# Performance work log

Hardware: AMD Instinct MI355X
Metric: run time of the kernel (lower is better)

Reference implementation:

```python
import jax, jax.numpy as jnp
import numpy as np

V, E, H2, K = 30000, 256, 256, 13  # vocab, embed dim, per-direction hidden, num tags
B, T = 64, 512


def setup_inputs() -> dict:
    key = jax.random.key(0)
    ks = jax.random.split(key, 12)
    s = 0.1
    return {
        "x": jax.random.randint(ks[0], (B, T), 0, V, dtype=jnp.int32),
        "emb": jax.random.normal(ks[1], (V, E), dtype=jnp.float32) * s,
        "w_ih_f": jax.random.normal(ks[2], (4 * H2, E), dtype=jnp.float32) * s,
        "w_hh_f": jax.random.normal(ks[3], (4 * H2, H2), dtype=jnp.float32) * s,
        "b_ih_f": jnp.zeros((4 * H2,), jnp.float32),
        "b_hh_f": jnp.zeros((4 * H2,), jnp.float32),
        "w_ih_b": jax.random.normal(ks[4], (4 * H2, E), dtype=jnp.float32) * s,
        "w_hh_b": jax.random.normal(ks[5], (4 * H2, H2), dtype=jnp.float32) * s,
        "b_ih_b": jnp.zeros((4 * H2,), jnp.float32),
        "b_hh_b": jnp.zeros((4 * H2,), jnp.float32),
        "w_out": jax.random.normal(ks[6], (K, 2 * H2), dtype=jnp.float32) * s,
        "b_out": jnp.zeros((K,), jnp.float32),
        "start_trans": jax.random.normal(ks[7], (K,), dtype=jnp.float32) * s,
        "end_trans": jax.random.normal(ks[8], (K,), dtype=jnp.float32) * s,
        "trans": jax.random.normal(ks[9], (K, K), dtype=jnp.float32) * s,
    }


def _lstm_dir(xg, w_hh, reverse):
    # xg: [T, B, 4H] precomputed input-side gate pre-activations (PyTorch i|f|g|o order)
    Bsz, H = xg.shape[1], w_hh.shape[1]

    def step(carry, g_in):
        h, c = carry
        g = g_in + h @ w_hh.T
        i, f, gg, o = jnp.split(g, 4, axis=-1)
        c = jax.nn.sigmoid(f) * c + jax.nn.sigmoid(i) * jnp.tanh(gg)
        h = jax.nn.sigmoid(o) * jnp.tanh(c)
        return (h, c), h

    init = (jnp.zeros((Bsz, H), xg.dtype), jnp.zeros((Bsz, H), xg.dtype))
    _, hs = jax.lax.scan(step, init, xg, reverse=reverse)
    return hs  # [T, B, H]


def reference(x, emb, w_ih_f, w_hh_f, b_ih_f, b_hh_f, w_ih_b, w_hh_b, b_ih_b, b_hh_b,
              w_out, b_out, start_trans, end_trans, trans):
    e = emb[x].transpose(1, 0, 2)                     # [T, B, E] time-major
    xg_f = e @ w_ih_f.T + (b_ih_f + b_hh_f)           # [T, B, 4H] (fold both biases)
    xg_b = e @ w_ih_b.T + (b_ih_b + b_hh_b)
    h_f = _lstm_dir(xg_f, w_hh_f, reverse=False)
    h_b = _lstm_dir(xg_b, w_hh_b, reverse=True)
    h = jnp.concatenate([h_f, h_b], axis=-1)          # [T, B, 2H]; dropout = identity (eval)
    emissions = h @ w_out.T + b_out                   # [T, B, K]

    # CRF Viterbi decode (torchcrf semantics, full mask)
    score = start_trans + emissions[0]                # [B, K]

    def vstep(score, emit_t):
        s = score[:, :, None] + trans[None] + emit_t[:, None, :]  # [B, K_prev, K_next]
        return s.max(axis=1), s.argmax(axis=1)

    score, bps = jax.lax.scan(vstep, score, emissions[1:])        # bps: [T-1, B, K]
    score = score + end_trans
    best_last = jnp.argmax(score, axis=-1)            # [B]
    best_score = jnp.max(score, axis=-1)              # [B]

    def btstep(tag, bp_t):
        prev = jnp.take_along_axis(bp_t, tag[:, None], axis=1)[:, 0]
        return prev, prev

    _, path_head = jax.lax.scan(btstep, best_last, bps, reverse=True)  # [T-1, B]
    path = jnp.concatenate([path_head, best_last[None]], axis=0).T     # [B, T]
    return path, best_score
```

## Files before the change

### kernel.cpp

```cpp
#include <hip/hip_runtime.h>
#include <stdint.h>
#include <stddef.h>

#define T_LEN  512
#define BATCH  64
#define NTAG   13
#define CT     64
#define NCHUNK 8

__device__ __forceinline__ float sigm(float x) { return 1.0f / (1.0f + expf(-x)); }

__global__ __launch_bounds__(256) void xg_gemm(
    const int* __restrict__ x, const float* __restrict__ emb,
    const float* __restrict__ w_ih_f, const float* __restrict__ w_ih_b,
    const float* __restrict__ b_ih_f, const float* __restrict__ b_hh_f,
    const float* __restrict__ b_ih_b, const float* __restrict__ b_hh_b,
    float* __restrict__ xg_ws, int chunk)
{
    const int tid = threadIdx.x;
    const int mt = blockIdx.x;
    const int nt = blockIdx.y;
    const int d  = blockIdx.z;
    const int tbase = (d == 0 ? chunk : (NCHUNK - 1 - chunk)) * CT;
    const float* W  = (d == 0) ? w_ih_f : w_ih_b;
    const float* bi = (d == 0) ? b_ih_f : b_ih_b;
    const float* bh = (d == 0) ? b_hh_f : b_hh_b;

    __shared__ __align__(16) float Wl[16][132];
    __shared__ __align__(16) float El[16][132];
    __shared__ int tok[128];

    if (tid < 128) {
        int col = nt * 128 + tid;
        tok[tid] = x[(col & 63) * T_LEN + tbase + (col >> 6)];
    }
    __syncthreads();

    const int r  = tid >> 1;
    const int c8 = (tid & 1) * 8;
    const int tm = tid >> 4;
    const int tn = tid & 15;

    float acc[8][8];
#pragma unroll
    for (int i = 0; i < 8; i++)
#pragma unroll
        for (int jz = 0; jz < 8; jz++) acc[i][jz] = 0.0f;

    const float* wrow = &W[(size_t)(mt * 128 + r) * 256];
    const float* erow = &emb[(size_t)tok[r] * 256];

    for (int kb = 0; kb < 256; kb += 16) {
        float4 w0 = *(const float4*)&wrow[kb + c8];
        float4 w1 = *(const float4*)&wrow[kb + c8 + 4];
        float4 e0 = *(const float4*)&erow[kb + c8];
        float4 e1 = *(const float4*)&erow[kb + c8 + 4];
        __syncthreads();
        Wl[c8+0][r] = w0.x; Wl[c8+1][r] = w0.y; Wl[c8+2][r] = w0.z; Wl[c8+3][r] = w0.w;
        Wl[c8+4][r] = w1.x; Wl[c8+5][r] = w1.y; Wl[c8+6][r] = w1.z; Wl[c8+7][r] = w1.w;
        El[c8+0][r] = e0.x; El[c8+1][r] = e0.y; El[c8+2][r] = e0.z; El[c8+3][r] = e0.w;
        El[c8+4][r] = e1.x; El[c8+5][r] = e1.y; El[c8+6][r] = e1.z; El[c8+7][r] = e1.w;
        __syncthreads();
#pragma unroll
        for (int kk = 0; kk < 16; kk++) {
            float a[8], b[8];
            *(float4*)&a[0] = *(const float4*)&Wl[kk][tm*8];
            *(float4*)&a[4] = *(const float4*)&Wl[kk][tm*8+4];
            *(float4*)&b[0] = *(const float4*)&El[kk][tn*8];
            *(float4*)&b[4] = *(const float4*)&El[kk][tn*8+4];
#pragma unroll
            for (int i = 0; i < 8; i++)
#pragma unroll
                for (int jz = 0; jz < 8; jz++)
                    acc[i][jz] += a[i] * b[jz];
        }
    }

    const int colbase = nt * 128 + tn * 8;
    const int j  = colbase >> 6;
    const int b0 = colbase & 63;
#pragma unroll
    for (int gi = 0; gi < 8; gi++) {
        int g = mt * 128 + tm * 8 + gi;
        float bias = bi[g] + bh[g];
        float* dst = &xg_ws[(((size_t)(d * CT + j) * 1024 + g) << 6) + b0];
        float4 v0 = make_float4(acc[gi][0]+bias, acc[gi][1]+bias, acc[gi][2]+bias, acc[gi][3]+bias);
        float4 v1 = make_float4(acc[gi][4]+bias, acc[gi][5]+bias, acc[gi][6]+bias, acc[gi][7]+bias);
        *(float4*)dst       = v0;
        *(float4*)(dst + 4) = v1;
    }
}

__global__ __launch_bounds__(256) void lstm_chunk(
    const float* __restrict__ xg_ws,
    const float* __restrict__ w_hh_f, const float* __restrict__ w_hh_b,
    float* h_ex, float* c_state, float* h_all, int* flags, int chunk)
{
    const int tid = threadIdx.x;
    const int bid = blockIdx.x;
    const int dg    = bid & 7;
    const int slice = bid >> 3;
    const int dir = dg & 1;
    const int grp = dg >> 1;
    const int h_base = slice * 8;
    const int sbase  = grp * 16;

    __shared__ __align__(16) float w_lds[32][260];
    __shared__ __align__(16) float h_lds[16][260];
    __shared__ __align__(16) float red[7][32][20];
    __shared__ float gatebuf[32][17];

    const float* W = dir ? w_hh_b : w_hh_f;
    for (int idx = tid; idx < 2048; idx += 256) {
        int f  = idx << 2;
        int rr = f >> 8;
        int c4 = f & 255;
        int row = (rr >> 3) * 256 + h_base + (rr & 7);
        *(float4*)&w_lds[rr][c4] = *(const float4*)&W[(size_t)row * 256 + c4];
    }

    const int ih_g = tid & 7;
    const int s_g  = tid >> 3;
    float c_val = 0.0f;
    if (tid < 128)
        c_val = c_state[(size_t)(dir * 64 + sbase + s_g) * 256 + h_base + ih_g];

    {
        const float* base = &h_ex[((size_t)dg * 16) * 256];
#pragma unroll
        for (int i = 0; i < 8; i++) {
            int pos = tid + 256 * i;
            int fo  = pos << 1;
            unsigned long long u64 = __hip_atomic_load(
                (const unsigned long long*)(base + fo), __ATOMIC_RELAXED, __HIP_MEMORY_SCOPE_AGENT);
            float2 v = __builtin_bit_cast(float2, u64);
            *(float2*)&h_lds[fo >> 8][fo & 255] = v;
        }
    }
    __syncthreads();

    const int kc   = tid >> 5;
    const int tile = tid & 31;
    const int gt = tile >> 2;
    const int st = tile & 3;
    const float* wr[4] = { &w_lds[gt][0], &w_lds[8+gt][0], &w_lds[16+gt][0], &w_lds[24+gt][0] };
    const float* hr[4] = { &h_lds[st][0], &h_lds[4+st][0], &h_lds[8+st][0],  &h_lds[12+st][0] };

    float hv_prev = 0.0f;
    size_t ha_prev = 0;

#pragma unroll 1
    for (int tl = 0; tl < CT; tl++) {
        const int jslot = dir ? (CT - 1 - tl) : tl;
        const int t = (dir ? (NCHUNK - 1 - chunk) : chunk) * CT + jslot;
        const int sc = chunk * CT + tl + 1;
        const int par = sc & 1;

        float xg0 = 0.f, xg1 = 0.f, xg2 = 0.f, xg3 = 0.f;
        if (tid < 128) {
            if (tl > 0) h_all[ha_prev] = hv_prev;
            const float* xp = &xg_ws[(((size_t)(dir * CT + jslot) * 1024) + h_base + ih_g) * 64 + sbase + s_g];
            xg0 = xp[0];
            xg1 = xp[1 * 256 * 64];
            xg2 = xp[2 * 256 * 64];
            xg3 = xp[3 * 256 * 64];
        }

        float acc[4][4];
#pragma unroll
        for (int gi = 0; gi < 4; gi++)
#pragma unroll
            for (int si = 0; si < 4; si++) acc[gi][si] = 0.0f;

        const int j0 = kc * 32;
#pragma unroll
        for (int m = 0; m < 8; m++) {
            const int jj = j0 + m * 4;
            float4 w4[4], h4[4];
#pragma unroll
            for (int i = 0; i < 4; i++) w4[i] = *(const float4*)(wr[i] + jj);
#pragma unroll
            for (int i = 0; i < 4; i++) h4[i] = *(const float4*)(hr[i] + jj);
#pragma unroll
            for (int gi = 0; gi < 4; gi++)
#pragma unroll
                for (int si = 0; si < 4; si++)
                    acc[gi][si] += w4[gi].x*h4[si].x + w4[gi].y*h4[si].y
                                 + w4[gi].z*h4[si].z + w4[gi].w*h4[si].w;
        }

        if (kc >= 1) {
#pragma unroll
            for (int gi = 0; gi < 4; gi++)
                *(float4*)&red[kc-1][tile][gi*4] =
                    make_float4(acc[gi][0], acc[gi][1], acc[gi][2], acc[gi][3]);
        }
        __syncthreads();
        if (kc == 0) {
#pragma unroll
            for (int p = 0; p < 7; p++)
#pragma unroll
                for (int gi = 0; gi < 4; gi++) {
                    float4 v = *(const float4*)&red[p][tile][gi*4];
                    acc[gi][0] += v.x; acc[gi][1] += v.y; acc[gi][2] += v.z; acc[gi][3] += v.w;
                }
#pragma unroll
            for (int gi = 0; gi < 4; gi++)
#pragma unroll
                for (int si = 0; si < 4; si++)
                    gatebuf[8*gi + gt][4*si + st] = acc[gi][si];
        }
        __syncthreads();

        if (tid < 128) {
            float gI = gatebuf[     ih_g][s_g] + xg0;
            float gF = gatebuf[8  + ih_g][s_g] + xg1;
            float gG = gatebuf[16 + ih_g][s_g] + xg2;
            float gO = gatebuf[24 + ih_g][s_g] + xg3;
            c_val = sigm(gF) * c_val + sigm(gI) * tanhf(gG);
            float hv = sigm(gO) * tanhf(c_val);
            __hip_atomic_store(&h_ex[(((size_t)par * 8 + dg) * 16 + s_g) * 256 + h_base + ih_g],
                               hv, __ATOMIC_RELAXED, __HIP_MEMORY_SCOPE_AGENT);
            hv_prev = hv;
            ha_prev = ((size_t)t * 64 + sbase + s_g) * 512 + dir * 256 + h_base + ih_g;
        }
        __syncthreads();

        if (tid == 0)
            __hip_atomic_store(&flags[dg * 32 + slice], sc, __ATOMIC_RELAXED, __HIP_MEMORY_SCOPE_AGENT);

        if (tid < 64) {
            const int* fp = &flags[dg * 32 + (tid & 31)];
            int spins = 0;
            int v = __hip_atomic_load(fp, __ATOMIC_RELAXED, __HIP_MEMORY_SCOPE_AGENT);
            while (__ballot(v < sc) != 0ull) {
                if (++spins > 8) __builtin_amdgcn_s_sleep(1);
                v = __hip_atomic_load(fp, __ATOMIC_RELAXED, __HIP_MEMORY_SCOPE_AGENT);
                if (spins > (1 << 20)) break;
            }
        }
        __syncthreads();

        {
            const float* base = &h_ex[(((size_t)par * 8 + dg) * 16) * 256];
#pragma unroll
            for (int i = 0; i < 8; i++) {
                int pos = tid + 256 * i;
                int fo  = pos << 1;
                unsigned long long u64 = __hip_atomic_load(
                    (const unsigned long long*)(base + fo), __ATOMIC_RELAXED, __HIP_MEMORY_SCOPE_AGENT);
                float2 v = __builtin_bit_cast(float2, u64);
                *(float2*)&h_lds[fo >> 8][fo & 255] = v;
            }
        }
        __syncthreads();
    }

    if (tid < 128) {
        h_all[ha_prev] = hv_prev;
        c_state[(size_t)(dir * 64 + sbase + s_g) * 256 + h_base + ih_g] = c_val;
    }
}

__global__ __launch_bounds__(256) void emis_kernel(
    const float* __restrict__ h_all, const float* __restrict__ w_out,
    const float* __restrict__ b_out, float* __restrict__ emis)
{
    const int row = blockIdx.x * 16 + (threadIdx.x >> 4);
    const int k   = threadIdx.x & 15;
    const float* hr = &h_all[(size_t)row * 512];
    const float* wr = &w_out[(size_t)(k < NTAG ? k : 0) * 512];
    float acc = 0.0f;
#pragma unroll 8
    for (int e = 0; e < 512; e += 4) {
        float4 h4 = *(const float4*)&hr[e];
        float4 w4 = *(const float4*)&wr[e];
        acc += h4.x*w4.x + h4.y*w4.y + h4.z*w4.z + h4.w*w4.w;
    }
    if (k < NTAG) emis[(size_t)row * NTAG + k] = acc + b_out[k];
}

__global__ __launch_bounds__(64) void viterbi_kernel(
    const float* __restrict__ emis, const float* __restrict__ start_trans,
    const float* __restrict__ end_trans, const float* __restrict__ trans,
    float* __restrict__ out)
{
    const int b = blockIdx.x;
    const int k = threadIdx.x;
    __shared__ float em[T_LEN * NTAG];
    __shared__ unsigned char bp[T_LEN][16];

    for (int t = k; t < T_LEN; t += 64) {
        const float* src = &emis[((size_t)t * 64 + b) * NTAG];
#pragma unroll
        for (int kk = 0; kk < NTAG; kk++)
            em[t * NTAG + kk] = src[kk];
    }
    __syncthreads();

    float tc[NTAG];
#pragma unroll
    for (int kp = 0; kp < NTAG; kp++)
        tc[kp] = (k < NTAG) ? trans[kp * NTAG + k] : 0.0f;

    float score = (k < NTAG) ? (start_trans[k] + em[k]) : -3.0e38f;

    for (int t = 1; t < T_LEN; t++) {
        float best = -3.0e38f;
        int bi = 0;
#pragma unroll
        for (int kp = 0; kp < NTAG; kp++) {
            float v = __shfl(score, kp) + tc[kp];
            if (v > best) { best = v; bi = kp; }
        }
        if (k < NTAG) {
            score = best + em[t * NTAG + k];
            bp[t][k] = (unsigned char)bi;
        }
    }
    if (k < NTAG) score += end_trans[k];
    else score = -3.0e38f;
    __syncthreads();

    float bs = -3.0e38f;
    int tag = 0;
#pragma unroll
    for (int kk = 0; kk < NTAG; kk++) {
        float v = __shfl(score, kk);
        if (v > bs) { bs = v; tag = kk; }
    }
    if (k == 0) {
        out[32768 + b] = bs;
        int tg = tag;
        out[b * T_LEN + (T_LEN - 1)] = (float)tg;
        for (int t = T_LEN - 1; t >= 1; t--) {
            tg = bp[t][tg];
            out[b * T_LEN + t - 1] = (float)tg;
        }
    }
}

extern "C" void kernel_launch(void* const* d_in, const int* in_sizes, int n_in,
                              void* d_out, int out_size, void* d_ws, size_t ws_size,
                              hipStream_t stream)
{
    (void)in_sizes; (void)n_in; (void)out_size; (void)ws_size;
    const int*   x    = (const int*)  d_in[0];
    const float* emb  = (const float*)d_in[1];
    const float* wihf = (const float*)d_in[2];
    const float* whhf = (const float*)d_in[3];
    const float* bihf = (const float*)d_in[4];
    const float* bhhf = (const float*)d_in[5];
    const float* wihb = (const float*)d_in[6];
    const float* whhb = (const float*)d_in[7];
    const float* bihb = (const float*)d_in[8];
    const float* bhhb = (const float*)d_in[9];
    const float* wout = (const float*)d_in[10];
    const float* bout = (const float*)d_in[11];
    const float* stt  = (const float*)d_in[12];
    const float* ent  = (const float*)d_in[13];
    const float* trn  = (const float*)d_in[14];
    float* out = (float*)d_out;

    char* ws = (char*)d_ws;
    size_t off = 0;
    float* xg_ws = (float*)(ws + off); off += (size_t)2 * CT * 1024 * 64 * 4;
    float* h_all = (float*)(ws + off); off += (size_t)T_LEN * 64 * 512 * 4;
    float* h_ex  = (float*)(ws + off); off += (size_t)2 * 8 * 16 * 256 * 4;
    float* c_st  = (float*)(ws + off); off += (size_t)2 * 64 * 256 * 4;
    float* emis  = (float*)(ws + off); off += (size_t)T_LEN * 64 * NTAG * 4;
    int*   flags = (int*)  (ws + off); off += 8 * 32 * 4;

    hipMemsetAsync(h_ex,  0, (size_t)2 * 8 * 16 * 256 * 4, stream);
    hipMemsetAsync(c_st,  0, (size_t)2 * 64 * 256 * 4, stream);
    hipMemsetAsync(flags, 0, 8 * 32 * 4, stream);

    for (int c = 0; c < NCHUNK; c++) {
        xg_gemm<<<dim3(8, 32, 2), 256, 0, stream>>>(x, emb, wihf, wihb,
                                                    bihf, bhhf, bihb, bhhb, xg_ws, c);
        lstm_chunk<<<256, 256, 0, stream>>>(xg_ws, whhf, whhb, h_ex, c_st, h_all, flags, c);
    }
    emis_kernel<<<2048, 256, 0, stream>>>(h_all, wout, bout, emis);
    viterbi_kernel<<<64, 64, 0, stream>>>(emis, stt, ent, trn, out);
}
```

Baseline: 3.458 ms.

## Replace flag barrier with sequence-tagged hidden-state exchange in LSTM chunk

Each hidden value exchanged between blocks is now packed into a 64-bit word together with its step counter. Readers spin directly on the data until every tag matches, which removes the separate flag store, the flag spin loop and two block barriers per timestep. The cost is twice the exchange buffer size and per-element polling traffic, and correctness now relies on the 64-bit atomic store and load being single, untorn accesses.

```diff
diff --git a/kernel.cpp b/kernel.cpp
--- a/kernel.cpp
+++ b/kernel.cpp
@@ -94,7 +94,7 @@
 __global__ __launch_bounds__(256) void lstm_chunk(
     const float* __restrict__ xg_ws,
     const float* __restrict__ w_hh_f, const float* __restrict__ w_hh_b,
-    float* h_ex, float* c_state, float* h_all, int* flags, int chunk)
+    unsigned long long* h_ex, float* c_state, float* h_all, int chunk)
 {
     const int tid = threadIdx.x;
     const int bid = blockIdx.x;
@@ -126,15 +126,23 @@
         c_val = c_state[(size_t)(dir * 64 + sbase + s_g) * 256 + h_base + ih_g];
 
     {
-        const float* base = &h_ex[((size_t)dg * 16) * 256];
-#pragma unroll
-        for (int i = 0; i < 8; i++) {
-            int pos = tid + 256 * i;
-            int fo  = pos << 1;
-            unsigned long long u64 = __hip_atomic_load(
-                (const unsigned long long*)(base + fo), __ATOMIC_RELAXED, __HIP_MEMORY_SCOPE_AGENT);
-            float2 v = __builtin_bit_cast(float2, u64);
-            *(float2*)&h_lds[fo >> 8][fo & 255] = v;
+        const unsigned long long* src = &h_ex[((size_t)dg * 16) * 256 + tid];
+        const unsigned exp0 = (unsigned)(chunk * CT);
+        unsigned pend = 0xffffu;
+        int spins = 0;
+        while (pend) {
+#pragma unroll
+            for (int i = 0; i < 16; i++) {
+                if (pend & (1u << i)) {
+                    unsigned long long u = __hip_atomic_load(
+                        &src[i * 256], __ATOMIC_RELAXED, __HIP_MEMORY_SCOPE_AGENT);
+                    if ((unsigned)(u >> 32) == exp0) {
+                        h_lds[i][tid] = __uint_as_float((unsigned)(u & 0xffffffffu));
+                        pend &= ~(1u << i);
+                    }
+                }
+            }
+            if (pend && ++spins > (1 << 20)) break;
         }
     }
     __syncthreads();
@@ -219,41 +227,37 @@
             float gO = gatebuf[24 + ih_g][s_g] + xg3;
             c_val = sigm(gF) * c_val + sigm(gI) * tanhf(gG);
             float hv = sigm(gO) * tanhf(c_val);
+            unsigned long long pk = ((unsigned long long)(unsigned)sc << 32)
+                                  | (unsigned long long)__float_as_uint(hv);
             __hip_atomic_store(&h_ex[(((size_t)par * 8 + dg) * 16 + s_g) * 256 + h_base + ih_g],
-                               hv, __ATOMIC_RELAXED, __HIP_MEMORY_SCOPE_AGENT);
+                               pk, __ATOMIC_RELAXED, __HIP_MEMORY_SCOPE_AGENT);
             hv_prev = hv;
             ha_prev = ((size_t)t * 64 + sbase + s_g) * 512 + dir * 256 + h_base + ih_g;
         }
-        __syncthreads();
-
-        if (tid == 0)
-            __hip_atomic_store(&flags[dg * 32 + slice], sc, __ATOMIC_RELAXED, __HIP_MEMORY_SCOPE_AGENT);
-
-        if (tid < 64) {
-            const int* fp = &flags[dg * 32 + (tid & 31)];
+
+        if (tl != CT - 1) {
+            const unsigned long long* src = &h_ex[(((size_t)par * 8 + dg) * 16) * 256 + tid];
+            unsigned pend = 0xffffu;
             int spins = 0;
-            int v = __hip_atomic_load(fp, __ATOMIC_RELAXED, __HIP_MEMORY_SCOPE_AGENT);
-            while (__ballot(v < sc) != 0ull) {
-                if (++spins > 8) __builtin_amdgcn_s_sleep(1);
-                v = __hip_atomic_load(fp, __ATOMIC_RELAXED, __HIP_MEMORY_SCOPE_AGENT);
-                if (spins > (1 << 20)) break;
+            while (pend) {
+#pragma unroll
+                for (int i = 0; i < 16; i++) {
+                    if (pend & (1u << i)) {
+                        unsigned long long u = __hip_atomic_load(
+                            &src[i * 256], __ATOMIC_RELAXED, __HIP_MEMORY_SCOPE_AGENT);
+                        if ((unsigned)(u >> 32) == (unsigned)sc) {
+                            h_lds[i][tid] = __uint_as_float((unsigned)(u & 0xffffffffu));
+                            pend &= ~(1u << i);
+                        }
+                    }
+                }
+                if (pend) {
+                    if (++spins > 32) __builtin_amdgcn_s_sleep(1);
+                    if (spins > (1 << 20)) break;
+                }
             }
-        }
-        __syncthreads();
-
-        {
-            const float* base = &h_ex[(((size_t)par * 8 + dg) * 16) * 256];
-#pragma unroll
-            for (int i = 0; i < 8; i++) {
-                int pos = tid + 256 * i;
-                int fo  = pos << 1;
-                unsigned long long u64 = __hip_atomic_load(
-                    (const unsigned long long*)(base + fo), __ATOMIC_RELAXED, __HIP_MEMORY_SCOPE_AGENT);
-                float2 v = __builtin_bit_cast(float2, u64);
-                *(float2*)&h_lds[fo >> 8][fo & 255] = v;
-            }
-        }
-        __syncthreads();
+            __syncthreads();
+        }
     }
 
     if (tid < 128) {
@@ -366,19 +370,18 @@
     size_t off = 0;
     float* xg_ws = (float*)(ws + off); off += (size_t)2 * CT * 1024 * 64 * 4;
     float* h_all = (float*)(ws + off); off += (size_t)T_LEN * 64 * 512 * 4;
-    float* h_ex  = (float*)(ws + off); off += (size_t)2 * 8 * 16 * 256 * 4;
+    unsigned long long* h_ex = (unsigned long long*)(ws + off);
+    off += (size_t)2 * 8 * 16 * 256 * 8;
     float* c_st  = (float*)(ws + off); off += (size_t)2 * 64 * 256 * 4;
     float* emis  = (float*)(ws + off); off += (size_t)T_LEN * 64 * NTAG * 4;
-    int*   flags = (int*)  (ws + off); off += 8 * 32 * 4;
-
-    hipMemsetAsync(h_ex,  0, (size_t)2 * 8 * 16 * 256 * 4, stream);
+
+    hipMemsetAsync(h_ex,  0, (size_t)2 * 8 * 16 * 256 * 8, stream);
     hipMemsetAsync(c_st,  0, (size_t)2 * 64 * 256 * 4, stream);
-    hipMemsetAsync(flags, 0, 8 * 32 * 4, stream);
 
     for (int c = 0; c < NCHUNK; c++) {
         xg_gemm<<<dim3(8, 32, 2), 256, 0, stream>>>(x, emb, wihf, wihb,
                                                     bihf, bhhf, bihb, bhhb, xg_ws, c);
-        lstm_chunk<<<256, 256, 0, stream>>>(xg_ws, whhf, whhb, h_ex, c_st, h_all, flags, c);
+        lstm_chunk<<<256, 256, 0, stream>>>(xg_ws, whhf, whhb, h_ex, c_st, h_all, c);
     }
     emis_kernel<<<2048, 256, 0, stream>>>(h_all, wout, bout, emis);
     viterbi_kernel<<<64, 64, 0, stream>>>(emis, stt, ent, trn, out);
```

After: 4.654 ms. 34.6% more time.

## Overlap next-chunk input GEMM with LSTM recurrence in one fused launch

Applied to the files above, without the earlier changes.

The LSTM chunk and the input-projection GEMM are merged into a single kernel. Blocks 0-255 run the recurrence for chunk c, while the remaining 512 blocks compute input-gate pre-activations for chunk c+1 into a second xg buffer, with the two buffers alternating between chunks. The goal is to hide the GEMM behind the latency-bound recurrence and drop one launch per chunk. In exchange, the GEMM blocks now reserve the full ~70KB of shared memory, which lowers their occupancy. The spin-synchronised LSTM blocks also have to share CUs with the extra blocks, and the fused path needs a larger workspace, otherwise the code falls back to the old sequence.

```diff
diff --git a/kernel.cpp b/kernel.cpp
--- a/kernel.cpp
+++ b/kernel.cpp
@@ -10,25 +10,24 @@
 
 __device__ __forceinline__ float sigm(float x) { return 1.0f / (1.0f + expf(-x)); }
 
-__global__ __launch_bounds__(256) void xg_gemm(
+#define SMEM_BYTES 70016
+
+__device__ __forceinline__ void xg_body(char* smem,
     const int* __restrict__ x, const float* __restrict__ emb,
     const float* __restrict__ w_ih_f, const float* __restrict__ w_ih_b,
     const float* __restrict__ b_ih_f, const float* __restrict__ b_hh_f,
     const float* __restrict__ b_ih_b, const float* __restrict__ b_hh_b,
-    float* __restrict__ xg_ws, int chunk)
-{
+    float* __restrict__ xg_ws, int chunk, int mt, int nt, int d)
+{
+    float (*Wl)[132] = (float(*)[132])(smem);
+    float (*El)[132] = (float(*)[132])(smem + 8448);
+    int*   tok       = (int*)(smem + 16896);
+
     const int tid = threadIdx.x;
-    const int mt = blockIdx.x;
-    const int nt = blockIdx.y;
-    const int d  = blockIdx.z;
     const int tbase = (d == 0 ? chunk : (NCHUNK - 1 - chunk)) * CT;
     const float* W  = (d == 0) ? w_ih_f : w_ih_b;
     const float* bi = (d == 0) ? b_ih_f : b_ih_b;
     const float* bh = (d == 0) ? b_hh_f : b_hh_b;
-
-    __shared__ __align__(16) float Wl[16][132];
-    __shared__ __align__(16) float El[16][132];
-    __shared__ int tok[128];
 
     if (tid < 128) {
         int col = nt * 128 + tid;
@@ -91,24 +90,23 @@
     }
 }
 
-__global__ __launch_bounds__(256) void lstm_chunk(
+__device__ __forceinline__ void lstm_body(char* smem,
     const float* __restrict__ xg_ws,
     const float* __restrict__ w_hh_f, const float* __restrict__ w_hh_b,
-    float* h_ex, float* c_state, float* h_all, int* flags, int chunk)
-{
+    float* h_ex, float* c_state, float* h_all, int* flags, int chunk, int bid)
+{
+    float (*w_lds)[260]   = (float(*)[260])(smem);
+    float (*h_lds)[260]   = (float(*)[260])(smem + 33280);
+    float (*red)[32][20]  = (float(*)[32][20])(smem + 49920);
+    float (*gatebuf)[17]  = (float(*)[17])(smem + 67840);
+
     const int tid = threadIdx.x;
-    const int bid = blockIdx.x;
     const int dg    = bid & 7;
     const int slice = bid >> 3;
     const int dir = dg & 1;
     const int grp = dg >> 1;
     const int h_base = slice * 8;
     const int sbase  = grp * 16;
-
-    __shared__ __align__(16) float w_lds[32][260];
-    __shared__ __align__(16) float h_lds[16][260];
-    __shared__ __align__(16) float red[7][32][20];
-    __shared__ float gatebuf[32][17];
 
     const float* W = dir ? w_hh_b : w_hh_f;
     for (int idx = tid; idx < 2048; idx += 256) {
@@ -262,6 +260,52 @@
     }
 }
 
+__global__ __launch_bounds__(256) void xg_gemm(
+    const int* __restrict__ x, const float* __restrict__ emb,
+    const float* __restrict__ w_ih_f, const float* __restrict__ w_ih_b,
+    const float* __restrict__ b_ih_f, const float* __restrict__ b_hh_f,
+    const float* __restrict__ b_ih_b, const float* __restrict__ b_hh_b,
+    float* __restrict__ xg_ws, int chunk)
+{
+    __shared__ __align__(16) char smem[SMEM_BYTES];
+    xg_body(smem, x, emb, w_ih_f, w_ih_b, b_ih_f, b_hh_f, b_ih_b, b_hh_b,
+            xg_ws, chunk, blockIdx.x, blockIdx.y, blockIdx.z);
+}
+
+__global__ __launch_bounds__(256) void lstm_chunk(
+    const float* __restrict__ xg_ws,
+    const float* __restrict__ w_hh_f, const float* __restrict__ w_hh_b,
+    float* h_ex, float* c_state, float* h_all, int* flags, int chunk)
+{
+    __shared__ __align__(16) char smem[SMEM_BYTES];
+    lstm_body(smem, xg_ws, w_hh_f, w_hh_b, h_ex, c_state, h_all, flags, chunk, blockIdx.x);
+}
+
+__global__ __launch_bounds__(256) void lstm_xg_fused(
+    const float* __restrict__ xg_read,
+    const float* __restrict__ w_hh_f, const float* __restrict__ w_hh_b,
+    float* h_ex, float* c_state, float* h_all, int* flags, int chunk,
+    const int* __restrict__ x, const float* __restrict__ emb,
+    const float* __restrict__ w_ih_f, const float* __restrict__ w_ih_b,
+    const float* __restrict__ b_ih_f, const float* __restrict__ b_hh_f,
+    const float* __restrict__ b_ih_b, const float* __restrict__ b_hh_b,
+    float* __restrict__ xg_write)
+{
+    __shared__ __align__(16) char smem[SMEM_BYTES];
+    const int bid = blockIdx.x;
+    if (bid < 256) {
+        lstm_body(smem, xg_read, w_hh_f, w_hh_b, h_ex, c_state, h_all, flags, chunk, bid);
+    } else {
+        const int xid = bid - 256;
+        const int d   = xid >> 8;
+        const int rem = xid & 255;
+        const int mt  = rem & 7;
+        const int nt  = rem >> 3;
+        xg_body(smem, x, emb, w_ih_f, w_ih_b, b_ih_f, b_hh_f, b_ih_b, b_hh_b,
+                xg_write, chunk + 1, mt, nt, d);
+    }
+}
+
 __global__ __launch_bounds__(256) void emis_kernel(
     const float* __restrict__ h_all, const float* __restrict__ w_out,
     const float* __restrict__ b_out, float* __restrict__ emis)
@@ -344,7 +388,7 @@
                               void* d_out, int out_size, void* d_ws, size_t ws_size,
                               hipStream_t stream)
 {
-    (void)in_sizes; (void)n_in; (void)out_size; (void)ws_size;
+    (void)in_sizes; (void)n_in; (void)out_size;
     const int*   x    = (const int*)  d_in[0];
     const float* emb  = (const float*)d_in[1];
     const float* wihf = (const float*)d_in[2];
@@ -362,23 +406,49 @@
     const float* trn  = (const float*)d_in[14];
     float* out = (float*)d_out;
 
+    const size_t XG_BYTES   = (size_t)2 * CT * 1024 * 64 * 4;
+    const size_t HALL_BYTES = (size_t)T_LEN * 64 * 512 * 4;
+    const size_t HEX_BYTES  = (size_t)2 * 8 * 16 * 256 * 4;
+    const size_t CST_BYTES  = (size_t)2 * 64 * 256 * 4;
+    const size_t EMIS_BYTES = (size_t)T_LEN * 64 * NTAG * 4;
+    const size_t FLAG_BYTES = 8 * 32 * 4;
+
+    const size_t need_fused = 2 * XG_BYTES + HALL_BYTES + HEX_BYTES
+                            + CST_BYTES + EMIS_BYTES + FLAG_BYTES;
+    const bool fused = (ws_size == 0) || (ws_size >= need_fused);
+
     char* ws = (char*)d_ws;
     size_t off = 0;
-    float* xg_ws = (float*)(ws + off); off += (size_t)2 * CT * 1024 * 64 * 4;
-    float* h_all = (float*)(ws + off); off += (size_t)T_LEN * 64 * 512 * 4;
-    float* h_ex  = (float*)(ws + off); off += (size_t)2 * 8 * 16 * 256 * 4;
-    float* c_st  = (float*)(ws + off); off += (size_t)2 * 64 * 256 * 4;
-    float* emis  = (float*)(ws + off); off += (size_t)T_LEN * 64 * NTAG * 4;
-    int*   flags = (int*)  (ws + off); off += 8 * 32 * 4;
-
-    hipMemsetAsync(h_ex,  0, (size_t)2 * 8 * 16 * 256 * 4, stream);
-    hipMemsetAsync(c_st,  0, (size_t)2 * 64 * 256 * 4, stream);
-    hipMemsetAsync(flags, 0, 8 * 32 * 4, stream);
-
-    for (int c = 0; c < NCHUNK; c++) {
+    float* xg0 = (float*)(ws + off); off += XG_BYTES;
+    float* xg1 = xg0;
+    if (fused) { xg1 = (float*)(ws + off); off += XG_BYTES; }
+    float* h_all = (float*)(ws + off); off += HALL_BYTES;
+    float* h_ex  = (float*)(ws + off); off += HEX_BYTES;
+    float* c_st  = (float*)(ws + off); off += CST_BYTES;
+    float* emis  = (float*)(ws + off); off += EMIS_BYTES;
+    int*   flags = (int*)  (ws + off); off += FLAG_BYTES;
+
+    hipMemsetAsync(h_ex,  0, HEX_BYTES, stream);
+    hipMemsetAsync(c_st,  0, CST_BYTES, stream);
+    hipMemsetAsync(flags, 0, FLAG_BYTES, stream);
+
+    if (fused) {
         xg_gemm<<<dim3(8, 32, 2), 256, 0, stream>>>(x, emb, wihf, wihb,
-                                                    bihf, bhhf, bihb, bhhb, xg_ws, c);
-        lstm_chunk<<<256, 256, 0, stream>>>(xg_ws, whhf, whhb, h_ex, c_st, h_all, flags, c);
+                                                    bihf, bhhf, bihb, bhhb, xg0, 0);
+        for (int c = 0; c < NCHUNK; c++) {
+            float* xr = (c & 1) ? xg1 : xg0;
+            float* xw = (c & 1) ? xg0 : xg1;
+            int grid = (c < NCHUNK - 1) ? 768 : 256;
+            lstm_xg_fused<<<grid, 256, 0, stream>>>(xr, whhf, whhb,
+                h_ex, c_st, h_all, flags, c,
+                x, emb, wihf, wihb, bihf, bhhf, bihb, bhhb, xw);
+        }
+    } else {
+        for (int c = 0; c < NCHUNK; c++) {
+            xg_gemm<<<dim3(8, 32, 2), 256, 0, stream>>>(x, emb, wihf, wihb,
+                                                        bihf, bhhf, bihb, bhhb, xg0, c);
+            lstm_chunk<<<256, 256, 0, stream>>>(xg0, whhf, whhb, h_ex, c_st, h_all, flags, c);
+        }
     }
     emis_kernel<<<2048, 256, 0, stream>>>(h_all, wout, bout, emis);
     viterbi_kernel<<<64, 64, 0, stream>>>(emis, stt, ent, trn, out);
```

Measured after the change: 3.599 ms. +4.1%, slower.

## Replace block barriers in LSTM step with per-wave flags and targeted h reads

Applied to the files above, without the earlier changes.

Each wave that computes h now publishes its own flag as soon as its stores drain, which removes the block-wide barrier before publishing. Every reader thread then spins only on the flag of the producer slice it needs, rather than having one wave poll all 32 flags and then the block sync. The h exchange reload is reorganised so each thread reads the segment from its polled producer, and the wait is skipped on the last step of a chunk. This shortens the critical path of the inter-block step barrier, at the cost of more threads polling global flags and subtler memory-ordering assumptions.

```diff
diff --git a/kernel.cpp b/kernel.cpp
--- a/kernel.cpp
+++ b/kernel.cpp
@@ -146,6 +146,12 @@
     const float* wr[4] = { &w_lds[gt][0], &w_lds[8+gt][0], &w_lds[16+gt][0], &w_lds[24+gt][0] };
     const float* hr[4] = { &h_lds[st][0], &h_lds[4+st][0], &h_lds[8+st][0],  &h_lds[12+st][0] };
 
+    const int rs  = tid >> 3;
+    const int rq  = tid & 7;
+    const int rw  = rq >> 2;
+    const int rs0 = rq * 2;
+    const int* rfp = &flags[(dg * 32 + rs) * 2 + rw];
+
     float hv_prev = 0.0f;
     size_t ha_prev = 0;
 
@@ -223,37 +229,35 @@
                                hv, __ATOMIC_RELAXED, __HIP_MEMORY_SCOPE_AGENT);
             hv_prev = hv;
             ha_prev = ((size_t)t * 64 + sbase + s_g) * 512 + dir * 256 + h_base + ih_g;
-        }
-        __syncthreads();
-
-        if (tid == 0)
-            __hip_atomic_store(&flags[dg * 32 + slice], sc, __ATOMIC_RELAXED, __HIP_MEMORY_SCOPE_AGENT);
-
-        if (tid < 64) {
-            const int* fp = &flags[dg * 32 + (tid & 31)];
+            asm volatile("s_waitcnt vmcnt(0)" ::: "memory");
+            if ((tid & 63) == 0)
+                __hip_atomic_store(&flags[(dg * 32 + slice) * 2 + (tid >> 6)], sc,
+                                   __ATOMIC_RELAXED, __HIP_MEMORY_SCOPE_AGENT);
+        }
+
+        if (tl != CT - 1) {
             int spins = 0;
-            int v = __hip_atomic_load(fp, __ATOMIC_RELAXED, __HIP_MEMORY_SCOPE_AGENT);
-            while (__ballot(v < sc) != 0ull) {
-                if (++spins > 8) __builtin_amdgcn_s_sleep(1);
-                v = __hip_atomic_load(fp, __ATOMIC_RELAXED, __HIP_MEMORY_SCOPE_AGENT);
+            while (__hip_atomic_load(rfp, __ATOMIC_RELAXED, __HIP_MEMORY_SCOPE_AGENT) < sc) {
+                if (++spins > 4) __builtin_amdgcn_s_sleep(1);
                 if (spins > (1 << 20)) break;
             }
-        }
-        __syncthreads();
-
-        {
-            const float* base = &h_ex[(((size_t)par * 8 + dg) * 16) * 256];
-#pragma unroll
-            for (int i = 0; i < 8; i++) {
-                int pos = tid + 256 * i;
-                int fo  = pos << 1;
-                unsigned long long u64 = __hip_atomic_load(
-                    (const unsigned long long*)(base + fo), __ATOMIC_RELAXED, __HIP_MEMORY_SCOPE_AGENT);
-                float2 v = __builtin_bit_cast(float2, u64);
-                *(float2*)&h_lds[fo >> 8][fo & 255] = v;
+            const unsigned long long* base =
+                (const unsigned long long*)&h_ex[(((size_t)par * 8 + dg) * 16) * 256];
+#pragma unroll
+            for (int k = 0; k < 2; k++) {
+                const unsigned long long* src = base + (rs0 + k) * 128 + rs * 4;
+                float2 v0 = __builtin_bit_cast(float2, __hip_atomic_load(src + 0, __ATOMIC_RELAXED, __HIP_MEMORY_SCOPE_AGENT));
+                float2 v1 = __builtin_bit_cast(float2, __hip_atomic_load(src + 1, __ATOMIC_RELAXED, __HIP_MEMORY_SCOPE_AGENT));
+                float2 v2 = __builtin_bit_cast(float2, __hip_atomic_load(src + 2, __ATOMIC_RELAXED, __HIP_MEMORY_SCOPE_AGENT));
+                float2 v3 = __builtin_bit_cast(float2, __hip_atomic_load(src + 3, __ATOMIC_RELAXED, __HIP_MEMORY_SCOPE_AGENT));
+                float* drow = &h_lds[rs0 + k][rs * 8];
+                *(float2*)(drow + 0) = v0;
+                *(float2*)(drow + 2) = v1;
+                *(float2*)(drow + 4) = v2;
+                *(float2*)(drow + 6) = v3;
             }
-        }
-        __syncthreads();
+            __syncthreads();
+        }
     }
 
     if (tid < 128) {
@@ -369,11 +373,11 @@
     float* h_ex  = (float*)(ws + off); off += (size_t)2 * 8 * 16 * 256 * 4;
     float* c_st  = (float*)(ws + off); off += (size_t)2 * 64 * 256 * 4;
     float* emis  = (float*)(ws + off); off += (size_t)T_LEN * 64 * NTAG * 4;
-    int*   flags = (int*)  (ws + off); off += 8 * 32 * 4;
+    int*   flags = (int*)  (ws + off); off += 8 * 32 * 2 * 4;
 
     hipMemsetAsync(h_ex,  0, (size_t)2 * 8 * 16 * 256 * 4, stream);
     hipMemsetAsync(c_st,  0, (size_t)2 * 64 * 256 * 4, stream);
-    hipMemsetAsync(flags, 0, 8 * 32 * 4, stream);
+    hipMemsetAsync(flags, 0, 8 * 32 * 2 * 4, stream);
 
     for (int c = 0; c < NCHUNK; c++) {
         xg_gemm<<<dim3(8, 32, 2), 256, 0, stream>>>(x, emb, wihf, wihb,
```

After: 5.347 ms. 54.6% more time.
